# Performance work log

Measured on AMD Instinct MI355X. Metric: run time of the kernel, lower is better.

The kernel has to match this reference:

```python
import jax, jax.numpy as jnp
import numpy as np

B, C_IN, C_OUT, N, T = 32, 64, 64, 1024, 16


def setup_inputs() -> dict:
    key = jax.random.key(0)
    k1, k2, k3, k4, k5 = jax.random.split(key, 5)
    x = jax.random.normal(k1, (B, C_IN, N, T), dtype=jnp.float32)
    adj = jax.random.uniform(k2, (N, N), dtype=jnp.float32)
    alpha = jax.random.normal(k3, (C_IN,), dtype=jnp.float32) * 0.1
    W_att = jax.random.normal(k4, (T, T), dtype=jnp.float32) * 0.1
    W_out = jax.random.normal(k5, (C_OUT, C_IN), dtype=jnp.float32) * 0.1
    return {"x": x, "adj": adj, "alpha": alpha, "W_att": W_att, "W_out": W_out}


def reference(x, adj, alpha, W_att, W_out):
    # x: [B, C_in, N, T]; adj: [N, N]
    # k = q = einsum('bint,i->bnt', x, alpha)
    k = jnp.einsum('bint,i->bnt', x, alpha)              # [B, N, T]
    # scores = k @ W @ q^T over timestep dim -> [B, N, N]
    scores = jnp.einsum('bnt,ts,bms->bnm', k, W_att, k)
    att = jax.nn.softmax(scores, axis=-1) * adj          # [B, N, N]
    # out = (att @ x.permute(3,0,2,1)) @ W_out.T, then permute back
    agg = jnp.einsum('bnm,bcmt->bcnt', att, x)           # [B, C_in, N, T]
    out = jnp.einsum('bcnt,oc->bont', agg, W_out)        # [B, C_out, N, T]
    return out
```

## Files before the change

### kernel.cpp

```cpp
#include <hip/hip_runtime.h>
#include <hip/hip_bf16.h>


typedef float  f32x4 __attribute__((ext_vector_type(4)));
typedef short  s16x8 __attribute__((ext_vector_type(8)));
typedef unsigned short u16x8 __attribute__((ext_vector_type(8)));

#define GLOAD_LDS16(g, l) __builtin_amdgcn_global_load_lds(                    \
    (const __attribute__((address_space(1))) void*)(g),                        \
    (__attribute__((address_space(3))) void*)(l), 16, 0, 0)

static __device__ __forceinline__ unsigned short f2bf(float f) {
    __hip_bfloat16 h = __float2bfloat16(f);
    return *reinterpret_cast<unsigned short*>(&h);
}

__global__ __launch_bounds__(256, 3) void kCM(const float* __restrict__ x,
                                              const float* __restrict__ Wout,
                                              const float* __restrict__ alpha,
                                              const float* __restrict__ Watt,
                                              unsigned short* __restrict__ Yt,
                                              float* __restrict__ kk_,
                                              float* __restrict__ kq_) {
    extern __shared__ char sm[];
    unsigned short* xtb = (unsigned short*)sm;
    unsigned short* Ys  = (unsigned short*)sm;
    unsigned short* Wb  = (unsigned short*)(sm + 36864);
    float* al   = (float*)(sm + 46080);
    float* wl   = (float*)(sm + 46336);
    float* kl   = (float*)(sm + 47424);
    float* kred = (float*)(sm + 48448);
    int tid = threadIdx.x;
    int b  = blockIdx.x >> 6;
    int mc = blockIdx.x & 63;
    int j0 = mc << 8;
    int m0 = mc << 4;
    int g = tid >> 6, lane = tid & 63;
    if (tid < 64) al[tid] = alpha[tid];
    wl[(tid >> 4) * 17 + (tid & 15)] = Watt[tid];
    #pragma unroll
    for (int it = 0; it < 16; ++it) {
        int idx = it * 256 + tid;
        Wb[(idx >> 6) * 72 + (idx & 63)] = f2bf(Wout[idx]);
    }
    __syncthreads();
    const float* xb = x + (size_t)b * (64 * 16384) + j0;
    float kp[4] = {0.f, 0.f, 0.f, 0.f};
    #pragma unroll
    for (int it = 0; it < 16; ++it) {
        int c = it * 4 + g;
        float4 v = *(const float4*)(xb + (size_t)c * 16384 + lane * 4);
        float a = al[c];
        kp[0] = fmaf(a, v.x, kp[0]);
        kp[1] = fmaf(a, v.y, kp[1]);
        kp[2] = fmaf(a, v.z, kp[2]);
        kp[3] = fmaf(a, v.w, kp[3]);
        ushort4 pk = make_ushort4(f2bf(v.x), f2bf(v.y), f2bf(v.z), f2bf(v.w));
        *(ushort4*)&xtb[c * 264 + lane * 4] = pk;
    }
    *(float4*)&kred[g * 256 + lane * 4] = make_float4(kp[0], kp[1], kp[2], kp[3]);
    __syncthreads();
    int l15 = lane & 15, lhi = lane >> 4;
    int jw = g << 6;
    s16x8 af[4][2], bfv[4][2];
    #pragma unroll
    for (int fro = 0; fro < 4; ++fro)
        #pragma unroll
        for (int ks = 0; ks < 2; ++ks)
            af[fro][ks] = *(const s16x8*)&Wb[(fro * 16 + l15) * 72 + ks * 32 + lhi * 8];
    #pragma unroll
    for (int fc = 0; fc < 4; ++fc)
        #pragma unroll
        for (int ks = 0; ks < 2; ++ks) {
            int jcol = jw + fc * 16 + l15;
            int cb = ks * 32 + lhi * 8;
            s16x8 t;
            #pragma unroll
            for (int e = 0; e < 8; ++e)
                t[e] = (short)xtb[(cb + e) * 264 + jcol];
            bfv[fc][ks] = t;
        }
    float kv = kred[tid] + kred[256 + tid] + kred[512 + tid] + kred[768 + tid];
    kl[tid] = kv;
    kk_[(size_t)b * 16384 + j0 + tid] = kv;
    __syncthreads();
    f32x4 acc[4][4] = {};
    #pragma unroll
    for (int ks = 0; ks < 2; ++ks)
        #pragma unroll
        for (int fc = 0; fc < 4; ++fc)
            #pragma unroll
            for (int fro = 0; fro < 4; ++fro)
                acc[fro][fc] = __builtin_amdgcn_mfma_f32_16x16x32_bf16(
                    af[fro][ks], bfv[fc][ks], acc[fro][fc], 0, 0, 0);
    {
        int ml = tid >> 4, tq = tid & 15;
        float q = 0.f;
        #pragma unroll
        for (int s = 0; s < 16; ++s) q = fmaf(kl[ml * 16 + s], wl[s * 17 + tq], q);
        kq_[(size_t)b * 16384 + j0 + tid] = q;
    }
    #pragma unroll
    for (int fro = 0; fro < 4; ++fro)
        #pragma unroll
        for (int fc = 0; fc < 4; ++fc) {
            int jl = jw + fc * 16 + l15;
            int o0 = fro * 16 + lhi * 4;
            ushort4 pk = make_ushort4(f2bf(acc[fro][fc][0]), f2bf(acc[fro][fc][1]),
                                      f2bf(acc[fro][fc][2]), f2bf(acc[fro][fc][3]));
            *(ushort4*)&Ys[jl * 72 + o0] = pk;
        }
    __syncthreads();
    #pragma unroll
    for (int it = 0; it < 4; ++it) {
        int r = it * 256 + tid;
        int o = r >> 4, t = r & 15;
        u16x8 v0, v1;
        #pragma unroll
        for (int q = 0; q < 8; ++q) {
            v0[q] = Ys[(q * 16 + t) * 72 + o];
            v1[q] = Ys[((q + 8) * 16 + t) * 72 + o];
        }
        unsigned short* dst = Yt + (((size_t)b << 10) + r) * 1024 + m0;
        *(u16x8*)dst = v0;
        *(u16x8*)(dst + 8) = v1;
    }
}

__global__ __launch_bounds__(256) void kBP(const float* __restrict__ kk_,
                                           const float* __restrict__ kq_,
                                           const float* __restrict__ adj,
                                           unsigned short* __restrict__ Pbf) {
    int tid = threadIdx.x;
    int b  = blockIdx.x >> 8;
    int n0 = (blockIdx.x & 255) * 4;
    __shared__ float kql[4][16];
    __shared__ float redm[4][4], reds[4][4];
    if (tid < 64)
        kql[tid >> 4][tid & 15] =
            kq_[((size_t)b * 1024 + n0 + (tid >> 4)) * 16 + (tid & 15)];
    __syncthreads();
    const float* kb = kk_ + (size_t)b * 16384;
    float kf[4][16];
    #pragma unroll
    for (int u = 0; u < 4; ++u) {
        const float* p = &kb[(size_t)(u * 256 + tid) * 16];
        #pragma unroll
        for (int s = 0; s < 16; ++s) kf[u][s] = p[s];
    }
    float sc[4][4];
    #pragma unroll
    for (int r = 0; r < 4; ++r)
        #pragma unroll
        for (int u = 0; u < 4; ++u) {
            float a = 0.f;
            #pragma unroll
            for (int s = 0; s < 16; ++s) a = fmaf(kql[r][s], kf[u][s], a);
            sc[r][u] = a;
        }
    float mx[4];
    #pragma unroll
    for (int r = 0; r < 4; ++r)
        mx[r] = fmaxf(fmaxf(sc[r][0], sc[r][1]), fmaxf(sc[r][2], sc[r][3]));
    #pragma unroll
    for (int off = 32; off; off >>= 1)
        #pragma unroll
        for (int r = 0; r < 4; ++r) mx[r] = fmaxf(mx[r], __shfl_xor(mx[r], off));
    int w = tid >> 6;
    if ((tid & 63) == 0)
        #pragma unroll
        for (int r = 0; r < 4; ++r) redm[w][r] = mx[r];
    __syncthreads();
    #pragma unroll
    for (int r = 0; r < 4; ++r)
        mx[r] = fmaxf(fmaxf(redm[0][r], redm[1][r]), fmaxf(redm[2][r], redm[3][r]));
    float e[4][4], se[4];
    #pragma unroll
    for (int r = 0; r < 4; ++r) {
        float s = 0.f;
        #pragma unroll
        for (int u = 0; u < 4; ++u) { e[r][u] = __expf(sc[r][u] - mx[r]); s += e[r][u]; }
        se[r] = s;
    }
    #pragma unroll
    for (int off = 32; off; off >>= 1)
        #pragma unroll
        for (int r = 0; r < 4; ++r) se[r] += __shfl_xor(se[r], off);
    if ((tid & 63) == 0)
        #pragma unroll
        for (int r = 0; r < 4; ++r) reds[w][r] = se[r];
    __syncthreads();
    float rrs[4];
    #pragma unroll
    for (int r = 0; r < 4; ++r)
        rrs[r] = 1.f / (reds[0][r] + reds[1][r] + reds[2][r] + reds[3][r]);
    #pragma unroll
    for (int r = 0; r < 4; ++r)
        #pragma unroll
        for (int u = 0; u < 4; ++u) {
            size_t m = (size_t)u * 256 + tid;
            float av = adj[(size_t)(n0 + r) * 1024 + m];
            Pbf[((size_t)b * 1024 + n0 + r) * 1024 + m] = f2bf(e[r][u] * rrs[r] * av);
        }
}

static __device__ __forceinline__ void stage_tile(const unsigned short* Pb,
                                                  const unsigned short* Yb,
                                                  unsigned short* lds, int buf,
                                                  int kt, int ww, int l) {
    int r8  = (l >> 3) & 7;
    int glc = ((l & 7) ^ r8) << 3;
    int k0  = kt << 6;
    unsigned short* base = lds + buf * 32768;
    #pragma unroll
    for (int s = 0; s < 4; ++s) {
        int row  = s * 64 + ww * 8;
        size_t g = ((size_t)(row + r8) << 10) + k0 + glc;
        GLOAD_LDS16(Pb + g, base + row * 64);
        GLOAD_LDS16(Yb + g, base + 16384 + row * 64);
    }
}

static __device__ __forceinline__ s16x8 frag_ld(const unsigned short* base,
                                                int R, int kc, int l7) {
    return *(const s16x8*)(base + R * 64 + ((kc ^ l7) << 3));
}

__global__ __launch_bounds__(512, 2) void kD(const unsigned short* __restrict__ P,
                                             const unsigned short* __restrict__ Yt,
                                             float* __restrict__ out) {
    extern __shared__ unsigned short lds[];
    int bid = blockIdx.x;
    int wg  = (bid & 7) * 64 + (bid >> 3);
    int b   = wg >> 4;
    int rem = wg & 15;
    int n0  = (rem & 3) << 8;
    int j0  = (rem >> 2) << 8;
    int tid = threadIdx.x;
    int l = tid & 63, ww = tid >> 6;
    int wr = ww >> 2, wc = ww & 3;
    int l15 = l & 15, lhi = l >> 4, l7 = l & 7;
    const unsigned short* Pb = P  + ((size_t)b << 20) + ((size_t)n0 << 10);
    const unsigned short* Yb = Yt + ((size_t)b << 20) + ((size_t)j0 << 10);

    f32x4 acc[8][4] = {};
    stage_tile(Pb, Yb, lds, 0, 0, ww, l);

    for (int kt = 0; kt < 16; ++kt) {
        int cur = kt & 1;
        const unsigned short* Ab = lds + cur * 32768;
        const unsigned short* Bb = Ab + 16384;
        if (kt < 15) {
            stage_tile(Pb, Yb, lds, cur ^ 1, kt + 1, ww, l);
            asm volatile("s_waitcnt vmcnt(8)" ::: "memory");
        } else {
            asm volatile("s_waitcnt vmcnt(0)" ::: "memory");
        }
        __builtin_amdgcn_s_barrier();
        s16x8 bf[4][2];
        #pragma unroll
        for (int q = 0; q < 4; ++q) {
            if (q == 0) {
                #pragma unroll
                for (int nj = 0; nj < 4; ++nj)
                    #pragma unroll
                    for (int ks = 0; ks < 2; ++ks)
                        bf[nj][ks] = frag_ld(Bb, wc * 64 + nj * 16 + l15,
                                             ks * 4 + lhi, l7);
            }
            s16x8 af[2][2];
            #pragma unroll
            for (int mi = 0; mi < 2; ++mi)
                #pragma unroll
                for (int ks = 0; ks < 2; ++ks)
                    af[mi][ks] = frag_ld(Ab, wr * 128 + (q * 2 + mi) * 16 + l15,
                                         ks * 4 + lhi, l7);
            __builtin_amdgcn_s_barrier();
            asm volatile("s_waitcnt lgkmcnt(0)" ::: "memory");
            __builtin_amdgcn_sched_barrier(0);
            __builtin_amdgcn_s_setprio(1);
            #pragma unroll
            for (int mi = 0; mi < 2; ++mi)
                #pragma unroll
                for (int nj = 0; nj < 4; ++nj)
                    #pragma unroll
                    for (int ks = 0; ks < 2; ++ks)
                        acc[q * 2 + mi][nj] = __builtin_amdgcn_mfma_f32_16x16x32_bf16(
                            af[mi][ks], bf[nj][ks], acc[q * 2 + mi][nj], 0, 0, 0);
            __builtin_amdgcn_s_setprio(0);
            if (q < 3) __builtin_amdgcn_s_barrier();
        }
        __builtin_amdgcn_s_barrier();
    }

    #pragma unroll
    for (int mi = 0; mi < 8; ++mi)
        #pragma unroll
        for (int nj = 0; nj < 4; ++nj) {
            int o  = (j0 >> 4) + wc * 4 + nj;
            int nb = n0 + wr * 128 + mi * 16 + lhi * 4;
            float* op = out + ((size_t)(b * 64 + o) << 14) + (size_t)nb * 16 + l15;
            #pragma unroll
            for (int q = 0; q < 4; ++q) op[q * 16] = acc[mi][nj][q];
        }
}

extern "C" void kernel_launch(void* const* d_in, const int* in_sizes, int n_in,
                              void* d_out, int out_size, void* d_ws, size_t ws_size,
                              hipStream_t stream) {
    const float* x     = (const float*)d_in[0];
    const float* adj   = (const float*)d_in[1];
    const float* alpha = (const float*)d_in[2];
    const float* Watt  = (const float*)d_in[3];
    const float* Wout  = (const float*)d_in[4];
    float* out = (float*)d_out;

    char* ws = (char*)d_ws;
    float* k  = (float*)ws;
    float* kq = (float*)(ws + 2097152);
    unsigned short* Pbf = (unsigned short*)(ws + 4194304);
    unsigned short* Yt  = (unsigned short*)(ws + 4194304 + 67108864);

    kCM<<<2048, 256, 52544, stream>>>(x, Wout, alpha, Watt, Yt, k, kq);
    kBP<<<8192, 256, 0, stream>>>(k, kq, adj, Pbf);
    kD <<<512, 512, 131072, stream>>>(Pbf, Yt, out);
}
```

Baseline: 194.6 us.

## Halve kCM tile to raise occupancy and remap block IDs across XCDs

```diff
diff --git a/kernel.cpp b/kernel.cpp
--- a/kernel.cpp
+++ b/kernel.cpp
@@ -15,7 +15,7 @@
     return *reinterpret_cast<unsigned short*>(&h);
 }
 
-__global__ __launch_bounds__(256, 3) void kCM(const float* __restrict__ x,
+__global__ __launch_bounds__(256, 4) void kCM(const float* __restrict__ x,
                                               const float* __restrict__ Wout,
                                               const float* __restrict__ alpha,
                                               const float* __restrict__ Watt,
@@ -25,17 +25,18 @@
     extern __shared__ char sm[];
     unsigned short* xtb = (unsigned short*)sm;
     unsigned short* Ys  = (unsigned short*)sm;
-    unsigned short* Wb  = (unsigned short*)(sm + 36864);
-    float* al   = (float*)(sm + 46080);
-    float* wl   = (float*)(sm + 46336);
-    float* kl   = (float*)(sm + 47424);
-    float* kred = (float*)(sm + 48448);
+    unsigned short* Wb  = (unsigned short*)(sm + 18432);
+    float* al   = (float*)(sm + 27648);
+    float* wl   = (float*)(sm + 27904);
+    float* kl   = (float*)(sm + 28992);
+    float* kred = (float*)(sm + 29504);
     int tid = threadIdx.x;
-    int b  = blockIdx.x >> 6;
-    int mc = blockIdx.x & 63;
-    int j0 = mc << 8;
-    int m0 = mc << 4;
-    int g = tid >> 6, lane = tid & 63;
+    int bid = blockIdx.x;
+    int wg  = (bid & 7) * 512 + (bid >> 3);
+    int b   = wg >> 7;
+    int mc  = wg & 127;
+    int j0 = mc << 7;
+    int m0 = mc << 3;
     if (tid < 64) al[tid] = alpha[tid];
     wl[(tid >> 4) * 17 + (tid & 15)] = Watt[tid];
     #pragma unroll
@@ -44,32 +45,34 @@
         Wb[(idx >> 6) * 72 + (idx & 63)] = f2bf(Wout[idx]);
     }
     __syncthreads();
+    int cg = tid >> 5, q = tid & 31;
     const float* xb = x + (size_t)b * (64 * 16384) + j0;
     float kp[4] = {0.f, 0.f, 0.f, 0.f};
     #pragma unroll
-    for (int it = 0; it < 16; ++it) {
-        int c = it * 4 + g;
-        float4 v = *(const float4*)(xb + (size_t)c * 16384 + lane * 4);
+    for (int it = 0; it < 8; ++it) {
+        int c = it * 8 + cg;
+        float4 v = *(const float4*)(xb + (size_t)c * 16384 + q * 4);
         float a = al[c];
         kp[0] = fmaf(a, v.x, kp[0]);
         kp[1] = fmaf(a, v.y, kp[1]);
         kp[2] = fmaf(a, v.z, kp[2]);
         kp[3] = fmaf(a, v.w, kp[3]);
         ushort4 pk = make_ushort4(f2bf(v.x), f2bf(v.y), f2bf(v.z), f2bf(v.w));
-        *(ushort4*)&xtb[c * 264 + lane * 4] = pk;
-    }
-    *(float4*)&kred[g * 256 + lane * 4] = make_float4(kp[0], kp[1], kp[2], kp[3]);
-    __syncthreads();
+        *(ushort4*)&xtb[c * 132 + q * 4] = pk;
+    }
+    *(float4*)&kred[cg * 128 + q * 4] = make_float4(kp[0], kp[1], kp[2], kp[3]);
+    __syncthreads();
+    int w = tid >> 6, lane = tid & 63;
     int l15 = lane & 15, lhi = lane >> 4;
-    int jw = g << 6;
-    s16x8 af[4][2], bfv[4][2];
+    int jw = w << 5;
+    s16x8 af[4][2], bfv[2][2];
     #pragma unroll
     for (int fro = 0; fro < 4; ++fro)
         #pragma unroll
         for (int ks = 0; ks < 2; ++ks)
             af[fro][ks] = *(const s16x8*)&Wb[(fro * 16 + l15) * 72 + ks * 32 + lhi * 8];
     #pragma unroll
-    for (int fc = 0; fc < 4; ++fc)
+    for (int fc = 0; fc < 2; ++fc)
         #pragma unroll
         for (int ks = 0; ks < 2; ++ks) {
             int jcol = jw + fc * 16 + l15;
@@ -77,33 +80,37 @@
             s16x8 t;
             #pragma unroll
             for (int e = 0; e < 8; ++e)
-                t[e] = (short)xtb[(cb + e) * 264 + jcol];
+                t[e] = (short)xtb[(cb + e) * 132 + jcol];
             bfv[fc][ks] = t;
         }
-    float kv = kred[tid] + kred[256 + tid] + kred[512 + tid] + kred[768 + tid];
-    kl[tid] = kv;
-    kk_[(size_t)b * 16384 + j0 + tid] = kv;
-    __syncthreads();
-    f32x4 acc[4][4] = {};
+    if (tid < 128) {
+        float kv = 0.f;
+        #pragma unroll
+        for (int g8 = 0; g8 < 8; ++g8) kv += kred[g8 * 128 + tid];
+        kl[tid] = kv;
+        kk_[(size_t)b * 16384 + j0 + tid] = kv;
+    }
+    __syncthreads();
+    f32x4 acc[4][2] = {};
     #pragma unroll
     for (int ks = 0; ks < 2; ++ks)
         #pragma unroll
-        for (int fc = 0; fc < 4; ++fc)
+        for (int fc = 0; fc < 2; ++fc)
             #pragma unroll
             for (int fro = 0; fro < 4; ++fro)
                 acc[fro][fc] = __builtin_amdgcn_mfma_f32_16x16x32_bf16(
                     af[fro][ks], bfv[fc][ks], acc[fro][fc], 0, 0, 0);
-    {
+    if (tid < 128) {
         int ml = tid >> 4, tq = tid & 15;
-        float q = 0.f;
-        #pragma unroll
-        for (int s = 0; s < 16; ++s) q = fmaf(kl[ml * 16 + s], wl[s * 17 + tq], q);
-        kq_[(size_t)b * 16384 + j0 + tid] = q;
+        float qv = 0.f;
+        #pragma unroll
+        for (int s = 0; s < 16; ++s) qv = fmaf(kl[ml * 16 + s], wl[s * 17 + tq], qv);
+        kq_[(size_t)b * 16384 + j0 + tid] = qv;
     }
     #pragma unroll
     for (int fro = 0; fro < 4; ++fro)
         #pragma unroll
-        for (int fc = 0; fc < 4; ++fc) {
+        for (int fc = 0; fc < 2; ++fc) {
             int jl = jw + fc * 16 + l15;
             int o0 = fro * 16 + lhi * 4;
             ushort4 pk = make_ushort4(f2bf(acc[fro][fc][0]), f2bf(acc[fro][fc][1]),
@@ -115,15 +122,11 @@
     for (int it = 0; it < 4; ++it) {
         int r = it * 256 + tid;
         int o = r >> 4, t = r & 15;
-        u16x8 v0, v1;
-        #pragma unroll
-        for (int q = 0; q < 8; ++q) {
-            v0[q] = Ys[(q * 16 + t) * 72 + o];
-            v1[q] = Ys[((q + 8) * 16 + t) * 72 + o];
-        }
+        u16x8 v0;
+        #pragma unroll
+        for (int q8 = 0; q8 < 8; ++q8) v0[q8] = Ys[(q8 * 16 + t) * 72 + o];
         unsigned short* dst = Yt + (((size_t)b << 10) + r) * 1024 + m0;
         *(u16x8*)dst = v0;
-        *(u16x8*)(dst + 8) = v1;
     }
 }
 
@@ -132,8 +135,10 @@
                                            const float* __restrict__ adj,
                                            unsigned short* __restrict__ Pbf) {
     int tid = threadIdx.x;
-    int b  = blockIdx.x >> 8;
-    int n0 = (blockIdx.x & 255) * 4;
+    int bid = blockIdx.x;
+    int wg  = (bid & 7) * 1024 + (bid >> 3);
+    int b  = wg >> 8;
+    int n0 = (wg & 255) * 4;
     __shared__ float kql[4][16];
     __shared__ float redm[4][4], reds[4][4];
     if (tid < 64)
@@ -321,7 +326,7 @@
     unsigned short* Pbf = (unsigned short*)(ws + 4194304);
     unsigned short* Yt  = (unsigned short*)(ws + 4194304 + 67108864);
 
-    kCM<<<2048, 256, 52544, stream>>>(x, Wout, alpha, Watt, Yt, k, kq);
+    kCM<<<4096, 256, 33600, stream>>>(x, Wout, alpha, Watt, Yt, k, kq);
     kBP<<<8192, 256, 0, stream>>>(k, kq, adj, Pbf);
     kD <<<512, 512, 131072, stream>>>(Pbf, Yt, out);
 }
```

Measured after the change: 196.2 us. No clear change (+0.8%).
